# Kernel tuning notes

Measured on AMD Instinct MI355X. Metric: run time of the kernel, lower is better.

Reference implementation:

```python
import jax, jax.numpy as jnp
import numpy as np

N = 50000
E = 800000
IN_DIM = 128
HIDDEN = 32
HEADS = 4
OUT_DIM = 64
NEG_SLOPE = 0.2


def _glorot(key, shape):
    fan_in, fan_out = shape[0], shape[-1]
    lim = jnp.sqrt(6.0 / (fan_in + fan_out))
    return jax.random.uniform(key, shape, jnp.float32, -lim, lim)


def setup_inputs() -> dict:
    key = jax.random.key(0)
    ks = jax.random.split(key, 16)
    x = jax.random.normal(ks[0], (N, IN_DIM), jnp.float32)
    edge_index = jax.random.randint(ks[1], (2, E), 0, N, jnp.int64)
    # layer 0: in_dim -> hidden, heads, concat
    W1 = _glorot(ks[2], (IN_DIM, HEADS * HIDDEN))
    a_src1 = _glorot(ks[3], (HEADS, HIDDEN))
    a_dst1 = _glorot(ks[4], (HEADS, HIDDEN))
    b1 = jnp.zeros((HEADS * HIDDEN,), jnp.float32)
    # layer 1: hidden*heads -> hidden, heads, concat
    W2 = _glorot(ks[5], (HEADS * HIDDEN, HEADS * HIDDEN))
    a_src2 = _glorot(ks[6], (HEADS, HIDDEN))
    a_dst2 = _glorot(ks[7], (HEADS, HIDDEN))
    b2 = jnp.zeros((HEADS * HIDDEN,), jnp.float32)
    # layer 2: hidden*heads -> out_dim, heads, concat=False (mean over heads)
    W3 = _glorot(ks[8], (HEADS * HIDDEN, HEADS * OUT_DIM))
    a_src3 = _glorot(ks[9], (HEADS, OUT_DIM))
    a_dst3 = _glorot(ks[10], (HEADS, OUT_DIM))
    b3 = jnp.zeros((OUT_DIM,), jnp.float32)
    return {"x": x, "edge_index": edge_index,
            "W1": W1, "a_src1": a_src1, "a_dst1": a_dst1, "b1": b1,
            "W2": W2, "a_src2": a_src2, "a_dst2": a_dst2, "b2": b2,
            "W3": W3, "a_src3": a_src3, "a_dst3": a_dst3, "b3": b3}


def gat_conv(x, src, dst, W, a_src, a_dst, bias, out_ch, concat):
    # linear projection, per-head view: [N, H, C]
    h = (x @ W).reshape(N, HEADS, out_ch)
    # per-node attention logits, gathered to edges: [E, H]
    alpha_src = jnp.einsum('nhc,hc->nh', h, a_src)
    alpha_dst = jnp.einsum('nhc,hc->nh', h, a_dst)
    e = jax.nn.leaky_relu(alpha_src[src] + alpha_dst[dst], NEG_SLOPE)
    # segment softmax over incoming edges of each dst node
    m = jax.ops.segment_max(e, dst, num_segments=N)  # [N, H]
    m = jnp.where(jnp.isfinite(m), m, 0.0)
    p = jnp.exp(e - m[dst])  # [E, H]
    denom = jax.ops.segment_sum(p, dst, num_segments=N)  # [N, H]
    alpha = p / (denom[dst] + 1e-16)
    # weighted scatter-add of source features: [N, H, C]
    out = jax.ops.segment_sum(h[src] * alpha[:, :, None], dst, num_segments=N)
    if concat:
        return out.reshape(N, HEADS * out_ch) + bias
    return out.mean(axis=1) + bias


def reference(x, edge_index, W1, a_src1, a_dst1, b1, W2, a_src2, a_dst2, b2,
              W3, a_src3, a_dst3, b3):
    src, dst = edge_index[0], edge_index[1]
    x = gat_conv(x, src, dst, W1, a_src1, a_dst1, b1, HIDDEN, True)
    x = gat_conv(x, src, dst, W2, a_src2, a_dst2, b2, HIDDEN, True)
    x = gat_conv(x, src, dst, W3, a_src3, a_dst3, b3, OUT_DIM, False)
    return x
```

## Files before the change

kernel.cpp:

```cpp
#include <hip/hip_runtime.h>
#include <hip/hip_fp16.h>
#include <math.h>

#define NNODES 50000
#define NEDGES 800000

typedef _Float16 half8 __attribute__((ext_vector_type(8)));
typedef float floatx4 __attribute__((ext_vector_type(4)));


__global__ void zero_i32(int* __restrict__ p, int n) {
    int i = blockIdx.x * 256 + threadIdx.x;
    if (i < n) p[i] = 0;
}

__global__ void hist_kernel(const int* __restrict__ dst, int* __restrict__ counts, int e) {
    int i = blockIdx.x * 256 + threadIdx.x;
    if (i < e) atomicAdd(&counts[dst[i]], 1);
}

__global__ void scan1_kernel(const int* __restrict__ counts, int* __restrict__ row_ptr,
                             int* __restrict__ bsums, int n) {
    __shared__ int s[256];
    int tid = threadIdx.x;
    int i = blockIdx.x * 256 + tid;
    int v = (i < n) ? counts[i] : 0;
    s[tid] = v;
    __syncthreads();
    #pragma unroll
    for (int o = 1; o < 256; o <<= 1) {
        int t = (tid >= o) ? s[tid - o] : 0;
        __syncthreads();
        s[tid] += t;
        __syncthreads();
    }
    if (i < n) row_ptr[i + 1] = s[tid];
    if (tid == 255) bsums[blockIdx.x] = s[255];
}

__global__ void scan2_kernel(int* __restrict__ bsums, int nb) {
    __shared__ int s[256];
    int tid = threadIdx.x;
    int v = (tid < nb) ? bsums[tid] : 0;
    s[tid] = v;
    __syncthreads();
    #pragma unroll
    for (int o = 1; o < 256; o <<= 1) {
        int t = (tid >= o) ? s[tid - o] : 0;
        __syncthreads();
        s[tid] += t;
        __syncthreads();
    }
    if (tid < nb) bsums[tid] = s[tid] - v;
}

__global__ void scan3_kernel(int* __restrict__ row_ptr, const int* __restrict__ bsums,
                             int* __restrict__ cursor, int n) {
    int i = blockIdx.x * 256 + threadIdx.x;
    if (i < n) {
        row_ptr[i + 1] += bsums[blockIdx.x];
        cursor[i] = 0;
    }
    if (i == 0) row_ptr[0] = 0;
}

__global__ void fill_kernel(const int* __restrict__ src, const int* __restrict__ dst,
                            const int* __restrict__ row_ptr, int* __restrict__ cursor,
                            int* __restrict__ csr_src, int e) {
    int i = blockIdx.x * 256 + threadIdx.x;
    if (i < e) {
        int d = dst[i];
        int pos = atomicAdd(&cursor[d], 1);
        csr_src[row_ptr[d] + pos] = src[i];
    }
}


template <int CH, bool AF32, int LAYER>
__global__ __launch_bounds__(256, 3) void gemm_mfma(const void* __restrict__ A_,
                                                    const float* __restrict__ Wf,
                                                    const float* __restrict__ a_src,
                                                    const float* __restrict__ a_dst,
                                                    __half* __restrict__ H,
                                                    float* __restrict__ asrc,
                                                    float* __restrict__ adst, int n, int M) {
    __shared__ __half As[128][136];
    __shared__ __half Ws[64][136];
    float* scrf = (float*)&As[0][0];
    int tid = threadIdx.x;
    int row0 = blockIdx.x * 128;
    int col0 = blockIdx.y * 64;

    if constexpr (AF32) {
        const float* Af = (const float*)A_;
        #pragma unroll
        for (int it = 0; it < 8; ++it) {
            int flat = tid + it * 256;
            int r = flat >> 4;
            int kq = (flat & 15) * 8;
            int gr = row0 + r;
            float4 v0 = {0.f, 0.f, 0.f, 0.f}, v1 = {0.f, 0.f, 0.f, 0.f};
            if (gr < n) {
                v0 = *(const float4*)&Af[(size_t)gr * 128 + kq];
                v1 = *(const float4*)&Af[(size_t)gr * 128 + kq + 4];
            }
            __half2 h0 = __floats2half2_rn(v0.x, v0.y);
            __half2 h1 = __floats2half2_rn(v0.z, v0.w);
            __half2 h2 = __floats2half2_rn(v1.x, v1.y);
            __half2 h3 = __floats2half2_rn(v1.z, v1.w);
            uint4 st = {*(unsigned*)&h0, *(unsigned*)&h1, *(unsigned*)&h2, *(unsigned*)&h3};
            *(uint4*)&As[r][kq] = st;
        }
    } else {
        const __half* Ah = (const __half*)A_;
        #pragma unroll
        for (int it = 0; it < 8; ++it) {
            int flat = tid + it * 256;
            int r = flat >> 4;
            int kq = (flat & 15) * 8;
            int gr = row0 + r;
            float4 v = {0.f, 0.f, 0.f, 0.f};
            if (gr < n) v = *(const float4*)&Ah[(size_t)gr * 128 + kq];
            *(float4*)&As[r][kq] = v;
        }
    }
    #pragma unroll
    for (int it = 0; it < 4; ++it) {
        int flat = tid + it * 256;
        int kp = flat >> 4;
        int c4 = (flat & 15) * 4;
        int k = kp * 2;
        float4 va = *(const float4*)&Wf[(size_t)k * M + col0 + c4];
        float4 vb = *(const float4*)&Wf[(size_t)(k + 1) * M + col0 + c4];
        *(__half2*)&Ws[c4 + 0][k] = __floats2half2_rn(va.x, vb.x);
        *(__half2*)&Ws[c4 + 1][k] = __floats2half2_rn(va.y, vb.y);
        *(__half2*)&Ws[c4 + 2][k] = __floats2half2_rn(va.z, vb.z);
        *(__half2*)&Ws[c4 + 3][k] = __floats2half2_rn(va.w, vb.w);
    }
    __syncthreads();

    int lane = tid & 63;
    int wid = tid >> 6;
    int wm = (wid >> 1) * 64;
    int wn = (wid & 1) * 32;
    int l15 = lane & 15;
    int l4 = lane >> 4;

    floatx4 acc[4][2];
    #pragma unroll
    for (int mf = 0; mf < 4; ++mf)
        #pragma unroll
        for (int nf = 0; nf < 2; ++nf) {
            floatx4 z = {0.f, 0.f, 0.f, 0.f};
            acc[mf][nf] = z;
        }

    #pragma unroll
    for (int ks = 0; ks < 4; ++ks) {
        int kb = ks * 32 + l4 * 8;
        half8 b0 = *(const half8*)&Ws[wn + l15][kb];
        half8 b1 = *(const half8*)&Ws[wn + 16 + l15][kb];
        #pragma unroll
        for (int mf = 0; mf < 4; ++mf) {
            half8 a = *(const half8*)&As[wm + mf * 16 + l15][kb];
            acc[mf][0] = __builtin_amdgcn_mfma_f32_16x16x32_f16(a, b0, acc[mf][0], 0, 0, 0);
            acc[mf][1] = __builtin_amdgcn_mfma_f32_16x16x32_f16(a, b1, acc[mf][1], 0, 0, 0);
        }
    }
    if constexpr (CH == 64) __syncthreads();

    #pragma unroll
    for (int mf = 0; mf < 4; ++mf)
        #pragma unroll
        for (int r = 0; r < 4; ++r) {
            int gr = row0 + wm + mf * 16 + l4 * 4 + r;
            if (gr < n) {
                H[(size_t)gr * M + col0 + wn + l15] = __float2half(acc[mf][0][r]);
                H[(size_t)gr * M + col0 + wn + 16 + l15] = __float2half(acc[mf][1][r]);
            }
        }

    int hw = (col0 + wn) / CH;
    int cb = (col0 + wn) % CH;
    float vs0 = a_src[hw * CH + cb + l15];
    float vs1 = a_src[hw * CH + cb + 16 + l15];
    float vd0 = a_dst[hw * CH + cb + l15];
    float vd1 = a_dst[hw * CH + cb + 16 + l15];

    #pragma unroll
    for (int mf = 0; mf < 4; ++mf)
        #pragma unroll
        for (int r = 0; r < 4; ++r) {
            float ss = acc[mf][0][r] * vs0 + acc[mf][1][r] * vs1;
            float sd = acc[mf][0][r] * vd0 + acc[mf][1][r] * vd1;
            #pragma unroll
            for (int o = 1; o < 16; o <<= 1) {
                ss += __shfl_xor(ss, o);
                sd += __shfl_xor(sd, o);
            }
            if (l15 == 0) {
                int ri = wm + mf * 16 + l4 * 4 + r;
                if constexpr (CH == 32) {
                    int gr = row0 + ri;
                    if (gr < n) {
                        asrc[(size_t)gr * 4 + hw] = ss;
                        adst[(size_t)gr * 4 + hw] = sd;
                    }
                } else {
                    scrf[((wid & 1) * 128 + ri) * 2 + 0] = ss;
                    scrf[((wid & 1) * 128 + ri) * 2 + 1] = sd;
                }
            }
        }
    if constexpr (CH == 64) {
        __syncthreads();
        if (tid < 128) {
            int gr = row0 + tid;
            if (gr < n) {
                int head = col0 / 64;
                asrc[(size_t)gr * 4 + head] = scrf[tid * 2 + 0] + scrf[(128 + tid) * 2 + 0];
                adst[(size_t)gr * 4 + head] = scrf[tid * 2 + 1] + scrf[(128 + tid) * 2 + 1];
            }
        }
    }
}


template <int CPL, bool MEAN, int LAYER>
__global__ __launch_bounds__(256) void aggregate_kernel(
    const __half* __restrict__ h, const float* __restrict__ asrc,
    const float* __restrict__ adst, const int* __restrict__ csr_src,
    const int* __restrict__ row_ptr, const float* __restrict__ bias,
    void* __restrict__ out_, int n) {
    __shared__ float lds[4][332];
    int wid = threadIdx.x >> 6;
    int lane = threadIdx.x & 63;
    int node = blockIdx.x * 4 + wid;
    if (node >= n) return;
    float* Wp = lds[wid];
    int* Ws = (int*)&lds[wid][264];
    int start = row_ptr[node];
    int end = row_ptr[node + 1];
    float4 ad = *(const float4*)&adst[(size_t)node * 4];

    int l32, head, j_off;
    if constexpr (CPL == 2) {
        l32 = lane & 31; head = l32 >> 3; j_off = lane >> 5;
    } else {
        l32 = lane; head = lane >> 4; j_off = 0;
    }
    int hoff = head * 66;

    float acc0 = 0.f, acc1 = 0.f, acc2 = 0.f, acc3 = 0.f, pw = 0.f;

    for (int base = start; base < end; base += 64) {
        int cnt = end - base;
        if (cnt > 64) cnt = 64;
        int s = 0;
        float4 pv = {0.f, 0.f, 0.f, 0.f};
        if (lane < cnt) {
            s = csr_src[base + lane];
            float4 a = *(const float4*)&asrc[(size_t)s * 4];
            float e0 = a.x + ad.x; e0 = (e0 > 0.f) ? e0 : 0.2f * e0;
            float e1 = a.y + ad.y; e1 = (e1 > 0.f) ? e1 : 0.2f * e1;
            float e2 = a.z + ad.z; e2 = (e2 > 0.f) ? e2 : 0.2f * e2;
            float e3 = a.w + ad.w; e3 = (e3 > 0.f) ? e3 : 0.2f * e3;
            pv.x = __expf(e0); pv.y = __expf(e1); pv.z = __expf(e2); pv.w = __expf(e3);
        }
        Wp[0 * 66 + lane] = pv.x;
        Wp[1 * 66 + lane] = pv.y;
        Wp[2 * 66 + lane] = pv.z;
        Wp[3 * 66 + lane] = pv.w;
        Ws[lane] = s;
        __builtin_amdgcn_wave_barrier();
        asm volatile("" ::: "memory");
        if constexpr (CPL == 2) {
            for (int jj = 0; jj < cnt; jj += 16) {
                float w[8]; int sa[8];
                #pragma unroll
                for (int u = 0; u < 8; ++u) {
                    int j = jj + 2 * u + j_off;
                    w[u] = Wp[hoff + j];
                    sa[u] = Ws[j];
                }
                float2 v[8];
                #pragma unroll
                for (int u = 0; u < 8; ++u)
                    v[u] = *(const float2*)(h + (size_t)sa[u] * 128 + l32 * 4);
                #pragma unroll
                for (int u = 0; u < 8; ++u) {
                    float2 f01 = __half22float2(((const __half2*)&v[u])[0]);
                    float2 f23 = __half22float2(((const __half2*)&v[u])[1]);
                    acc0 += w[u] * f01.x;
                    acc1 += w[u] * f01.y;
                    acc2 += w[u] * f23.x;
                    acc3 += w[u] * f23.y;
                    pw += w[u];
                }
            }
        } else {
            for (int jj = 0; jj < cnt; jj += 8) {
                float w[8]; int sa[8];
                #pragma unroll
                for (int u = 0; u < 8; ++u) {
                    int j = jj + u;
                    w[u] = Wp[hoff + j];
                    sa[u] = Ws[j];
                }
                float2 v[8];
                #pragma unroll
                for (int u = 0; u < 8; ++u)
                    v[u] = *(const float2*)(h + (size_t)sa[u] * 256 + lane * 4);
                #pragma unroll
                for (int u = 0; u < 8; ++u) {
                    float2 f01 = __half22float2(((const __half2*)&v[u])[0]);
                    float2 f23 = __half22float2(((const __half2*)&v[u])[1]);
                    acc0 += w[u] * f01.x;
                    acc1 += w[u] * f01.y;
                    acc2 += w[u] * f23.x;
                    acc3 += w[u] * f23.y;
                    pw += w[u];
                }
            }
        }
        __builtin_amdgcn_wave_barrier();
        asm volatile("" ::: "memory");
    }

    if constexpr (!MEAN) {
        acc0 += __shfl_xor(acc0, 32);
        acc1 += __shfl_xor(acc1, 32);
        acc2 += __shfl_xor(acc2, 32);
        acc3 += __shfl_xor(acc3, 32);
        pw += __shfl_xor(pw, 32);
        if (lane < 32) {
            float inv = 1.f / (pw + 1e-16f);
            float4 b = *(const float4*)&bias[l32 * 4];
            __half* out = (__half*)out_;
            __half2 ha = __floats2half2_rn(acc0 * inv + b.x, acc1 * inv + b.y);
            __half2 hb = __floats2half2_rn(acc2 * inv + b.z, acc3 * inv + b.w);
            uint2 st = {*(unsigned int*)&ha, *(unsigned int*)&hb};
            *(uint2*)&out[(size_t)node * 128 + l32 * 4] = st;
        }
    } else {
        float inv = 1.f / (pw + 1e-16f);
        float r0 = acc0 * inv, r1 = acc1 * inv, r2 = acc2 * inv, r3 = acc3 * inv;
        r0 += __shfl_xor(r0, 16); r0 += __shfl_xor(r0, 32);
        r1 += __shfl_xor(r1, 16); r1 += __shfl_xor(r1, 32);
        r2 += __shfl_xor(r2, 16); r2 += __shfl_xor(r2, 32);
        r3 += __shfl_xor(r3, 16); r3 += __shfl_xor(r3, 32);
        if (lane < 16) {
            float* out = (float*)out_;
            float4 b = *(const float4*)&bias[lane * 4];
            float4 o;
            o.x = 0.25f * r0 + b.x;
            o.y = 0.25f * r1 + b.y;
            o.z = 0.25f * r2 + b.z;
            o.w = 0.25f * r3 + b.w;
            *(float4*)&out[(size_t)node * 64 + lane * 4] = o;
        }
    }
}


extern "C" void kernel_launch(void* const* d_in, const int* in_sizes, int n_in,
                              void* d_out, int out_size, void* d_ws, size_t ws_size,
                              hipStream_t stream) {
    const float* x = (const float*)d_in[0];
    const int* ei = (const int*)d_in[1];
    const int* src = ei;
    const int* dst = ei + NEDGES;
    const float* W1 = (const float*)d_in[2];
    const float* as1 = (const float*)d_in[3];
    const float* ad1 = (const float*)d_in[4];
    const float* b1 = (const float*)d_in[5];
    const float* W2 = (const float*)d_in[6];
    const float* as2 = (const float*)d_in[7];
    const float* ad2 = (const float*)d_in[8];
    const float* b2 = (const float*)d_in[9];
    const float* W3 = (const float*)d_in[10];
    const float* as3 = (const float*)d_in[11];
    const float* ad3 = (const float*)d_in[12];
    const float* b3 = (const float*)d_in[13];

    char* ws = (char*)d_ws;
    size_t off = 0;
    auto take = [&](size_t bytes) -> char* {
        char* p = ws + off;
        off = (off + bytes + 255) & ~(size_t)255;
        return p;
    };
    int* csr = (int*)take((size_t)NEDGES * 4);
    int* row_ptr = (int*)take((size_t)(NNODES + 1) * 4);
    int* counts = (int*)take((size_t)NNODES * 4);
    int* cursor = (int*)take((size_t)NNODES * 4);
    int* bsums = (int*)take(1024 * 4);
    float* asrc = (float*)take((size_t)NNODES * 4 * 4);
    float* adst = (float*)take((size_t)NNODES * 4 * 4);
    __half* hbuf = (__half*)take((size_t)NNODES * 256 * 2);
    __half* buf1h = (__half*)take((size_t)NNODES * 128 * 2);
    float* outp = (float*)d_out;

    int nbN = (NNODES + 255) / 256;
    int nbE = (NEDGES + 255) / 256;
    int gnodeAgg = (NNODES + 3) / 4;

    zero_i32<<<nbN, 256, 0, stream>>>(counts, NNODES);
    hist_kernel<<<nbE, 256, 0, stream>>>(dst, counts, NEDGES);
    scan1_kernel<<<nbN, 256, 0, stream>>>(counts, row_ptr, bsums, NNODES);
    scan2_kernel<<<1, 256, 0, stream>>>(bsums, nbN);
    scan3_kernel<<<nbN, 256, 0, stream>>>(row_ptr, bsums, cursor, NNODES);
    fill_kernel<<<nbE, 256, 0, stream>>>(src, dst, row_ptr, cursor, csr, NEDGES);

    dim3 gA((NNODES + 127) / 128, 2);
    dim3 gB((NNODES + 127) / 128, 4);

    gemm_mfma<32, true, 1><<<gA, 256, 0, stream>>>(x, W1, as1, ad1, hbuf, asrc, adst, NNODES, 128);
    aggregate_kernel<2, false, 1><<<gnodeAgg, 256, 0, stream>>>(hbuf, asrc, adst, csr, row_ptr, b1, buf1h, NNODES);

    gemm_mfma<32, false, 2><<<gA, 256, 0, stream>>>(buf1h, W2, as2, ad2, hbuf, asrc, adst, NNODES, 128);
    aggregate_kernel<2, false, 2><<<gnodeAgg, 256, 0, stream>>>(hbuf, asrc, adst, csr, row_ptr, b2, buf1h, NNODES);

    gemm_mfma<64, false, 3><<<gB, 256, 0, stream>>>(buf1h, W3, as3, ad3, hbuf, asrc, adst, NNODES, 256);
    aggregate_kernel<4, true, 3><<<gnodeAgg, 256, 0, stream>>>(hbuf, asrc, adst, csr, row_ptr, b3, outp, NNODES);
}
```

Baseline: 287.2 us.

## Bucket CSR edges by source chunk within each destination row

The CSR build now histograms edges into (destination, source>>12) bins and uses a two-level prefix scan plus a row-pointer extraction kernel. Within each destination row, source indices are therefore grouped by 4096-node chunk. The aim is more local gathers of source features in the aggregation kernels. In exchange, preprocessing now works over about 650k bins and launches several more kernels.

```diff
diff --git a/kernel.cpp b/kernel.cpp
--- a/kernel.cpp
+++ b/kernel.cpp
@@ -4,6 +4,8 @@
 
 #define NNODES 50000
 #define NEDGES 800000
+#define NCHUNK 13
+#define NB2 (NNODES * NCHUNK)
 
 typedef _Float16 half8 __attribute__((ext_vector_type(8)));
 typedef float floatx4 __attribute__((ext_vector_type(4)));
@@ -14,12 +16,13 @@
     if (i < n) p[i] = 0;
 }
 
-__global__ void hist_kernel(const int* __restrict__ dst, int* __restrict__ counts, int e) {
+__global__ void hist2_kernel(const int* __restrict__ src, const int* __restrict__ dst,
+                             int* __restrict__ cnt2, int e) {
     int i = blockIdx.x * 256 + threadIdx.x;
-    if (i < e) atomicAdd(&counts[dst[i]], 1);
-}
-
-__global__ void scan1_kernel(const int* __restrict__ counts, int* __restrict__ row_ptr,
+    if (i < e) atomicAdd(&cnt2[dst[i] * NCHUNK + (src[i] >> 12)], 1);
+}
+
+__global__ void scan1_kernel(const int* __restrict__ counts, int* __restrict__ out,
                              int* __restrict__ bsums, int n) {
     __shared__ int s[256];
     int tid = threadIdx.x;
@@ -34,7 +37,7 @@
         s[tid] += t;
         __syncthreads();
     }
-    if (i < n) row_ptr[i + 1] = s[tid];
+    if (i < n) out[i + 1] = s[tid];
     if (tid == 255) bsums[blockIdx.x] = s[255];
 }
 
@@ -54,24 +57,31 @@
     if (tid < nb) bsums[tid] = s[tid] - v;
 }
 
-__global__ void scan3_kernel(int* __restrict__ row_ptr, const int* __restrict__ bsums,
+__global__ void scan3_kernel(int* __restrict__ out, const int* __restrict__ bsums,
                              int* __restrict__ cursor, int n) {
     int i = blockIdx.x * 256 + threadIdx.x;
     if (i < n) {
-        row_ptr[i + 1] += bsums[blockIdx.x];
+        out[i + 1] += bsums[blockIdx.x];
         cursor[i] = 0;
     }
-    if (i == 0) row_ptr[0] = 0;
-}
-
-__global__ void fill_kernel(const int* __restrict__ src, const int* __restrict__ dst,
-                            const int* __restrict__ row_ptr, int* __restrict__ cursor,
-                            int* __restrict__ csr_src, int e) {
+    if (i == 0) out[0] = 0;
+}
+
+__global__ void rowptr_kernel(const int* __restrict__ cp, int* __restrict__ row_ptr) {
+    int i = blockIdx.x * 256 + threadIdx.x;
+    if (i < NNODES) row_ptr[i] = cp[i * NCHUNK];
+    if (i == NNODES) row_ptr[NNODES] = NEDGES;
+}
+
+__global__ void fill2_kernel(const int* __restrict__ src, const int* __restrict__ dst,
+                             const int* __restrict__ cp, int* __restrict__ cursor,
+                             int* __restrict__ csr_src, int e) {
     int i = blockIdx.x * 256 + threadIdx.x;
     if (i < e) {
-        int d = dst[i];
-        int pos = atomicAdd(&cursor[d], 1);
-        csr_src[row_ptr[d] + pos] = src[i];
+        int s_ = src[i];
+        int b = dst[i] * NCHUNK + (s_ >> 12);
+        int pos = atomicAdd(&cursor[b], 1);
+        csr_src[cp[b] + pos] = s_;
     }
 }
 
@@ -392,25 +402,32 @@
     };
     int* csr = (int*)take((size_t)NEDGES * 4);
     int* row_ptr = (int*)take((size_t)(NNODES + 1) * 4);
-    int* counts = (int*)take((size_t)NNODES * 4);
-    int* cursor = (int*)take((size_t)NNODES * 4);
-    int* bsums = (int*)take(1024 * 4);
+    int* cnt2 = (int*)take((size_t)NB2 * 4);
+    int* cp = (int*)take((size_t)(NB2 + 1) * 4);
+    int* cursor2 = (int*)take((size_t)NB2 * 4);
+    int* bs1 = (int*)take(2608 * 4);
+    int* bs1s = (int*)take(2609 * 4);
+    int* bs2 = (int*)take(64 * 4);
     float* asrc = (float*)take((size_t)NNODES * 4 * 4);
     float* adst = (float*)take((size_t)NNODES * 4 * 4);
     __half* hbuf = (__half*)take((size_t)NNODES * 256 * 2);
     __half* buf1h = (__half*)take((size_t)NNODES * 128 * 2);
     float* outp = (float*)d_out;
 
-    int nbN = (NNODES + 255) / 256;
+    int nbB = (NB2 + 255) / 256;
     int nbE = (NEDGES + 255) / 256;
+    int nb1 = (2540 + 255) / 256;
     int gnodeAgg = (NNODES + 3) / 4;
 
-    zero_i32<<<nbN, 256, 0, stream>>>(counts, NNODES);
-    hist_kernel<<<nbE, 256, 0, stream>>>(dst, counts, NEDGES);
-    scan1_kernel<<<nbN, 256, 0, stream>>>(counts, row_ptr, bsums, NNODES);
-    scan2_kernel<<<1, 256, 0, stream>>>(bsums, nbN);
-    scan3_kernel<<<nbN, 256, 0, stream>>>(row_ptr, bsums, cursor, NNODES);
-    fill_kernel<<<nbE, 256, 0, stream>>>(src, dst, row_ptr, cursor, csr, NEDGES);
+    zero_i32<<<nbB, 256, 0, stream>>>(cnt2, NB2);
+    hist2_kernel<<<nbE, 256, 0, stream>>>(src, dst, cnt2, NEDGES);
+    scan1_kernel<<<nbB, 256, 0, stream>>>(cnt2, cp, bs1, NB2);
+    scan1_kernel<<<nb1, 256, 0, stream>>>(bs1, bs1s, bs2, 2540);
+    scan2_kernel<<<1, 256, 0, stream>>>(bs2, nb1);
+    scan3_kernel<<<nb1, 256, 0, stream>>>(bs1s, bs2, cursor2, 2540);
+    scan3_kernel<<<nbB, 256, 0, stream>>>(cp, bs1s, cursor2, NB2);
+    rowptr_kernel<<<(NNODES + 256) / 256, 256, 0, stream>>>(cp, row_ptr);
+    fill2_kernel<<<nbE, 256, 0, stream>>>(src, dst, cp, cursor2, csr, NEDGES);
 
     dim3 gA((NNODES + 127) / 128, 2);
     dim3 gB((NNODES + 127) / 128, 4);
```

After: 294.4 us. +2.5%, slower.

## Reorder layer-3 GAT as aggregate-then-project using precomputed attention vectors

Applied to the files above, without the earlier changes.

Layer 3 now computes attention logits directly from the 128-dim input with a precombined W3·a vector, skipping the 256-wide projection. It then aggregates the 128-dim input features per head into a 512-wide buffer, and finishes with a single GEMM against a reshaped W3 that also folds in the head mean and bias. The aim is to shrink the per-edge gather width in the last layer (128 fp16 instead of 256 per source) and drop the wide projection. In exchange it writes and reads a 50000x512 fp16 intermediate, adds small weight-prep kernels each call, and changes the fp16 rounding order.

```diff
diff --git a/kernel.cpp b/kernel.cpp
--- a/kernel.cpp
+++ b/kernel.cpp
@@ -75,18 +75,79 @@
     }
 }
 
-
-template <int CH, bool AF32, int LAYER>
+__global__ void prep_v_kernel(const float* __restrict__ W3, const float* __restrict__ as3,
+                              const float* __restrict__ ad3, float* __restrict__ Vs,
+                              float* __restrict__ Vd) {
+    int id = blockIdx.x * 256 + threadIdx.x;
+    if (id >= 1024) return;
+    int which = id >> 9;
+    int rem = id & 511;
+    int k = rem >> 2;
+    int hd = rem & 3;
+    const float* av = which ? ad3 : as3;
+    float s = 0.f;
+    #pragma unroll 8
+    for (int c = 0; c < 64; ++c)
+        s += W3[(size_t)k * 256 + hd * 64 + c] * av[hd * 64 + c];
+    (which ? Vd : Vs)[hd * 128 + k] = s;
+}
+
+__global__ void prep_wr_kernel(const float* __restrict__ W3, __half* __restrict__ Wr) {
+    int id = blockIdx.x * 256 + threadIdx.x;
+    if (id >= 64 * 512) return;
+    int c = id >> 9;
+    int rem = id & 511;
+    int hd = rem >> 7;
+    int k = rem & 127;
+    Wr[(size_t)c * 512 + hd * 128 + k] = __float2half(W3[(size_t)k * 256 + hd * 64 + c]);
+}
+
+__global__ __launch_bounds__(256) void alpha3_kernel(const __half* __restrict__ A,
+                                                     const float* __restrict__ Vs,
+                                                     const float* __restrict__ Vd,
+                                                     float* __restrict__ asrc,
+                                                     float* __restrict__ adst, int n) {
+    int wid = threadIdx.x >> 6;
+    int lane = threadIdx.x & 63;
+    int node = blockIdx.x * 4 + wid;
+    if (node >= n) return;
+    unsigned raw = *(const unsigned*)(A + (size_t)node * 128 + lane * 2);
+    float2 f = __half22float2(*(const __half2*)&raw);
+    float ss[4], sd[4];
+    #pragma unroll
+    for (int hd = 0; hd < 4; ++hd) {
+        ss[hd] = f.x * Vs[hd * 128 + lane * 2] + f.y * Vs[hd * 128 + lane * 2 + 1];
+        sd[hd] = f.x * Vd[hd * 128 + lane * 2] + f.y * Vd[hd * 128 + lane * 2 + 1];
+    }
+    #pragma unroll
+    for (int o = 1; o < 64; o <<= 1) {
+        #pragma unroll
+        for (int hd = 0; hd < 4; ++hd) {
+            ss[hd] += __shfl_xor(ss[hd], o);
+            sd[hd] += __shfl_xor(sd[hd], o);
+        }
+    }
+    if (lane == 0) {
+        #pragma unroll
+        for (int hd = 0; hd < 4; ++hd) {
+            asrc[(size_t)node * 4 + hd] = ss[hd];
+            adst[(size_t)node * 4 + hd] = sd[hd];
+        }
+    }
+}
+
+
+template <bool AF32, int LAYER>
 __global__ __launch_bounds__(256, 3) void gemm_mfma(const void* __restrict__ A_,
                                                     const float* __restrict__ Wf,
                                                     const float* __restrict__ a_src,
                                                     const float* __restrict__ a_dst,
                                                     __half* __restrict__ H,
                                                     float* __restrict__ asrc,
-                                                    float* __restrict__ adst, int n, int M) {
+                                                    float* __restrict__ adst, int n) {
+    const int M = 128, CH = 32;
     __shared__ __half As[128][136];
     __shared__ __half Ws[64][136];
-    float* scrf = (float*)&As[0][0];
     int tid = threadIdx.x;
     int row0 = blockIdx.x * 128;
     int col0 = blockIdx.y * 64;
@@ -167,7 +228,6 @@
             acc[mf][1] = __builtin_amdgcn_mfma_f32_16x16x32_f16(a, b1, acc[mf][1], 0, 0, 0);
         }
     }
-    if constexpr (CH == 64) __syncthreads();
 
     #pragma unroll
     for (int mf = 0; mf < 4; ++mf)
@@ -181,11 +241,10 @@
         }
 
     int hw = (col0 + wn) / CH;
-    int cb = (col0 + wn) % CH;
-    float vs0 = a_src[hw * CH + cb + l15];
-    float vs1 = a_src[hw * CH + cb + 16 + l15];
-    float vd0 = a_dst[hw * CH + cb + l15];
-    float vd1 = a_dst[hw * CH + cb + 16 + l15];
+    float vs0 = a_src[hw * CH + l15];
+    float vs1 = a_src[hw * CH + 16 + l15];
+    float vd0 = a_dst[hw * CH + l15];
+    float vd1 = a_dst[hw * CH + 16 + l15];
 
     #pragma unroll
     for (int mf = 0; mf < 4; ++mf)
@@ -198,40 +257,21 @@
                 ss += __shfl_xor(ss, o);
                 sd += __shfl_xor(sd, o);
             }
-            if (l15 == 0) {
-                int ri = wm + mf * 16 + l4 * 4 + r;
-                if constexpr (CH == 32) {
-                    int gr = row0 + ri;
-                    if (gr < n) {
-                        asrc[(size_t)gr * 4 + hw] = ss;
-                        adst[(size_t)gr * 4 + hw] = sd;
-                    }
-                } else {
-                    scrf[((wid & 1) * 128 + ri) * 2 + 0] = ss;
-                    scrf[((wid & 1) * 128 + ri) * 2 + 1] = sd;
-                }
-            }
-        }
-    if constexpr (CH == 64) {
-        __syncthreads();
-        if (tid < 128) {
-            int gr = row0 + tid;
-            if (gr < n) {
-                int head = col0 / 64;
-                asrc[(size_t)gr * 4 + head] = scrf[tid * 2 + 0] + scrf[(128 + tid) * 2 + 0];
-                adst[(size_t)gr * 4 + head] = scrf[tid * 2 + 1] + scrf[(128 + tid) * 2 + 1];
-            }
-        }
-    }
-}
-
-
-template <int CPL, bool MEAN, int LAYER>
+            int gr = row0 + wm + mf * 16 + l4 * 4 + r;
+            if (l15 == 0 && gr < n) {
+                asrc[(size_t)gr * 4 + hw] = ss;
+                adst[(size_t)gr * 4 + hw] = sd;
+            }
+        }
+}
+
+
+template <int LAYER>
 __global__ __launch_bounds__(256) void aggregate_kernel(
     const __half* __restrict__ h, const float* __restrict__ asrc,
     const float* __restrict__ adst, const int* __restrict__ csr_src,
     const int* __restrict__ row_ptr, const float* __restrict__ bias,
-    void* __restrict__ out_, int n) {
+    __half* __restrict__ out, int n) {
     __shared__ float lds[4][332];
     int wid = threadIdx.x >> 6;
     int lane = threadIdx.x & 63;
@@ -243,12 +283,7 @@
     int end = row_ptr[node + 1];
     float4 ad = *(const float4*)&adst[(size_t)node * 4];
 
-    int l32, head, j_off;
-    if constexpr (CPL == 2) {
-        l32 = lane & 31; head = l32 >> 3; j_off = lane >> 5;
-    } else {
-        l32 = lane; head = lane >> 4; j_off = 0;
-    }
+    int l32 = lane & 31, head = l32 >> 3, j_off = lane >> 5;
     int hoff = head * 66;
 
     float acc0 = 0.f, acc1 = 0.f, acc2 = 0.f, acc3 = 0.f, pw = 0.f;
@@ -274,92 +309,198 @@
         Ws[lane] = s;
         __builtin_amdgcn_wave_barrier();
         asm volatile("" ::: "memory");
-        if constexpr (CPL == 2) {
-            for (int jj = 0; jj < cnt; jj += 16) {
-                float w[8]; int sa[8];
-                #pragma unroll
-                for (int u = 0; u < 8; ++u) {
-                    int j = jj + 2 * u + j_off;
-                    w[u] = Wp[hoff + j];
-                    sa[u] = Ws[j];
-                }
-                float2 v[8];
-                #pragma unroll
-                for (int u = 0; u < 8; ++u)
-                    v[u] = *(const float2*)(h + (size_t)sa[u] * 128 + l32 * 4);
-                #pragma unroll
-                for (int u = 0; u < 8; ++u) {
-                    float2 f01 = __half22float2(((const __half2*)&v[u])[0]);
-                    float2 f23 = __half22float2(((const __half2*)&v[u])[1]);
-                    acc0 += w[u] * f01.x;
-                    acc1 += w[u] * f01.y;
-                    acc2 += w[u] * f23.x;
-                    acc3 += w[u] * f23.y;
-                    pw += w[u];
-                }
-            }
-        } else {
-            for (int jj = 0; jj < cnt; jj += 8) {
-                float w[8]; int sa[8];
-                #pragma unroll
-                for (int u = 0; u < 8; ++u) {
-                    int j = jj + u;
-                    w[u] = Wp[hoff + j];
-                    sa[u] = Ws[j];
-                }
-                float2 v[8];
-                #pragma unroll
-                for (int u = 0; u < 8; ++u)
-                    v[u] = *(const float2*)(h + (size_t)sa[u] * 256 + lane * 4);
-                #pragma unroll
-                for (int u = 0; u < 8; ++u) {
-                    float2 f01 = __half22float2(((const __half2*)&v[u])[0]);
-                    float2 f23 = __half22float2(((const __half2*)&v[u])[1]);
-                    acc0 += w[u] * f01.x;
-                    acc1 += w[u] * f01.y;
-                    acc2 += w[u] * f23.x;
-                    acc3 += w[u] * f23.y;
-                    pw += w[u];
-                }
+        for (int jj = 0; jj < cnt; jj += 16) {
+            float w[8]; int sa[8];
+            #pragma unroll
+            for (int u = 0; u < 8; ++u) {
+                int j = jj + 2 * u + j_off;
+                w[u] = Wp[hoff + j];
+                sa[u] = Ws[j];
+            }
+            float2 v[8];
+            #pragma unroll
+            for (int u = 0; u < 8; ++u)
+                v[u] = *(const float2*)(h + (size_t)sa[u] * 128 + l32 * 4);
+            #pragma unroll
+            for (int u = 0; u < 8; ++u) {
+                float2 f01 = __half22float2(((const __half2*)&v[u])[0]);
+                float2 f23 = __half22float2(((const __half2*)&v[u])[1]);
+                acc0 += w[u] * f01.x;
+                acc1 += w[u] * f01.y;
+                acc2 += w[u] * f23.x;
+                acc3 += w[u] * f23.y;
+                pw += w[u];
             }
         }
         __builtin_amdgcn_wave_barrier();
         asm volatile("" ::: "memory");
     }
 
-    if constexpr (!MEAN) {
-        acc0 += __shfl_xor(acc0, 32);
-        acc1 += __shfl_xor(acc1, 32);
-        acc2 += __shfl_xor(acc2, 32);
-        acc3 += __shfl_xor(acc3, 32);
-        pw += __shfl_xor(pw, 32);
-        if (lane < 32) {
-            float inv = 1.f / (pw + 1e-16f);
-            float4 b = *(const float4*)&bias[l32 * 4];
-            __half* out = (__half*)out_;
-            __half2 ha = __floats2half2_rn(acc0 * inv + b.x, acc1 * inv + b.y);
-            __half2 hb = __floats2half2_rn(acc2 * inv + b.z, acc3 * inv + b.w);
-            uint2 st = {*(unsigned int*)&ha, *(unsigned int*)&hb};
-            *(uint2*)&out[(size_t)node * 128 + l32 * 4] = st;
-        }
-    } else {
+    acc0 += __shfl_xor(acc0, 32);
+    acc1 += __shfl_xor(acc1, 32);
+    acc2 += __shfl_xor(acc2, 32);
+    acc3 += __shfl_xor(acc3, 32);
+    pw += __shfl_xor(pw, 32);
+    if (lane < 32) {
         float inv = 1.f / (pw + 1e-16f);
-        float r0 = acc0 * inv, r1 = acc1 * inv, r2 = acc2 * inv, r3 = acc3 * inv;
-        r0 += __shfl_xor(r0, 16); r0 += __shfl_xor(r0, 32);
-        r1 += __shfl_xor(r1, 16); r1 += __shfl_xor(r1, 32);
-        r2 += __shfl_xor(r2, 16); r2 += __shfl_xor(r2, 32);
-        r3 += __shfl_xor(r3, 16); r3 += __shfl_xor(r3, 32);
-        if (lane < 16) {
-            float* out = (float*)out_;
-            float4 b = *(const float4*)&bias[lane * 4];
-            float4 o;
-            o.x = 0.25f * r0 + b.x;
-            o.y = 0.25f * r1 + b.y;
-            o.z = 0.25f * r2 + b.z;
-            o.w = 0.25f * r3 + b.w;
-            *(float4*)&out[(size_t)node * 64 + lane * 4] = o;
-        }
-    }
+        float4 b = *(const float4*)&bias[l32 * 4];
+        __half2 ha = __floats2half2_rn(acc0 * inv + b.x, acc1 * inv + b.y);
+        __half2 hb = __floats2half2_rn(acc2 * inv + b.z, acc3 * inv + b.w);
+        uint2 st = {*(unsigned int*)&ha, *(unsigned int*)&hb};
+        *(uint2*)&out[(size_t)node * 128 + l32 * 4] = st;
+    }
+}
+
+
+__global__ __launch_bounds__(256) void aggregate_x_kernel(
+    const __half* __restrict__ A, const float* __restrict__ asrc,
+    const float* __restrict__ adst, const int* __restrict__ csr_src,
+    const int* __restrict__ row_ptr, __half* __restrict__ S, int n) {
+    __shared__ float lds[4][320];
+    int wid = threadIdx.x >> 6;
+    int lane = threadIdx.x & 63;
+    int node = blockIdx.x * 4 + wid;
+    if (node >= n) return;
+    float* Wp4 = lds[wid];
+    int* Ws = (int*)&lds[wid][256];
+    int start = row_ptr[node];
+    int end = row_ptr[node + 1];
+    float4 ad = *(const float4*)&adst[(size_t)node * 4];
+
+    float a00 = 0.f, a01 = 0.f, a10 = 0.f, a11 = 0.f;
+    float a20 = 0.f, a21 = 0.f, a30 = 0.f, a31 = 0.f;
+    float4 psum = {0.f, 0.f, 0.f, 0.f};
+
+    for (int base = start; base < end; base += 64) {
+        int cnt = end - base;
+        if (cnt > 64) cnt = 64;
+        int s = 0;
+        float4 pv = {0.f, 0.f, 0.f, 0.f};
+        if (lane < cnt) {
+            s = csr_src[base + lane];
+            float4 a = *(const float4*)&asrc[(size_t)s * 4];
+            float e0 = a.x + ad.x; e0 = (e0 > 0.f) ? e0 : 0.2f * e0;
+            float e1 = a.y + ad.y; e1 = (e1 > 0.f) ? e1 : 0.2f * e1;
+            float e2 = a.z + ad.z; e2 = (e2 > 0.f) ? e2 : 0.2f * e2;
+            float e3 = a.w + ad.w; e3 = (e3 > 0.f) ? e3 : 0.2f * e3;
+            pv.x = __expf(e0); pv.y = __expf(e1); pv.z = __expf(e2); pv.w = __expf(e3);
+            psum.x += pv.x; psum.y += pv.y; psum.z += pv.z; psum.w += pv.w;
+        }
+        *(float4*)&Wp4[lane * 4] = pv;
+        Ws[lane] = s;
+        __builtin_amdgcn_wave_barrier();
+        asm volatile("" ::: "memory");
+        for (int jj = 0; jj < cnt; jj += 8) {
+            int sa[8];
+            #pragma unroll
+            for (int u = 0; u < 8; ++u) sa[u] = Ws[jj + u];
+            unsigned raw[8];
+            #pragma unroll
+            for (int u = 0; u < 8; ++u)
+                raw[u] = *(const unsigned*)(A + (size_t)sa[u] * 128 + lane * 2);
+            #pragma unroll
+            for (int u = 0; u < 8; ++u) {
+                float4 p = *(const float4*)&Wp4[(jj + u) * 4];
+                float2 f = __half22float2(*(const __half2*)&raw[u]);
+                a00 += p.x * f.x; a01 += p.x * f.y;
+                a10 += p.y * f.x; a11 += p.y * f.y;
+                a20 += p.z * f.x; a21 += p.z * f.y;
+                a30 += p.w * f.x; a31 += p.w * f.y;
+            }
+        }
+        __builtin_amdgcn_wave_barrier();
+        asm volatile("" ::: "memory");
+    }
+
+    #pragma unroll
+    for (int o = 1; o < 64; o <<= 1) {
+        psum.x += __shfl_xor(psum.x, o);
+        psum.y += __shfl_xor(psum.y, o);
+        psum.z += __shfl_xor(psum.z, o);
+        psum.w += __shfl_xor(psum.w, o);
+    }
+    float s0 = 0.25f / (psum.x + 1e-16f);
+    float s1 = 0.25f / (psum.y + 1e-16f);
+    float s2 = 0.25f / (psum.z + 1e-16f);
+    float s3 = 0.25f / (psum.w + 1e-16f);
+    size_t sb = (size_t)node * 512 + lane * 2;
+    *(__half2*)&S[sb + 0 * 128] = __floats2half2_rn(a00 * s0, a01 * s0);
+    *(__half2*)&S[sb + 1 * 128] = __floats2half2_rn(a10 * s1, a11 * s1);
+    *(__half2*)&S[sb + 2 * 128] = __floats2half2_rn(a20 * s2, a21 * s2);
+    *(__half2*)&S[sb + 3 * 128] = __floats2half2_rn(a30 * s3, a31 * s3);
+}
+
+
+__global__ __launch_bounds__(256, 3) void post_gemm(const __half* __restrict__ S,
+                                                    const __half* __restrict__ Wr,
+                                                    const float* __restrict__ b3,
+                                                    float* __restrict__ out, int n) {
+    __shared__ __half As[128][136];
+    __shared__ __half Ws[64][136];
+    int tid = threadIdx.x;
+    int row0 = blockIdx.x * 128;
+    int lane = tid & 63;
+    int wid = tid >> 6;
+    int wm = (wid >> 1) * 64;
+    int wn = (wid & 1) * 32;
+    int l15 = lane & 15;
+    int l4 = lane >> 4;
+
+    floatx4 acc[4][2];
+    #pragma unroll
+    for (int mf = 0; mf < 4; ++mf)
+        #pragma unroll
+        for (int nf = 0; nf < 2; ++nf) {
+            floatx4 z = {0.f, 0.f, 0.f, 0.f};
+            acc[mf][nf] = z;
+        }
+
+    for (int kb = 0; kb < 512; kb += 128) {
+        #pragma unroll
+        for (int it = 0; it < 8; ++it) {
+            int flat = tid + it * 256;
+            int r = flat >> 4;
+            int kq = (flat & 15) * 8;
+            int gr = row0 + r;
+            float4 v = {0.f, 0.f, 0.f, 0.f};
+            if (gr < n) v = *(const float4*)&S[(size_t)gr * 512 + kb + kq];
+            *(float4*)&As[r][kq] = v;
+        }
+        #pragma unroll
+        for (int it = 0; it < 4; ++it) {
+            int flat = tid + it * 256;
+            int r = flat >> 4;
+            int kq = (flat & 15) * 8;
+            *(float4*)&Ws[r][kq] = *(const float4*)&Wr[(size_t)r * 512 + kb + kq];
+        }
+        __syncthreads();
+        #pragma unroll
+        for (int ks = 0; ks < 4; ++ks) {
+            int kk = ks * 32 + l4 * 8;
+            half8 b0 = *(const half8*)&Ws[wn + l15][kk];
+            half8 b1 = *(const half8*)&Ws[wn + 16 + l15][kk];
+            #pragma unroll
+            for (int mf = 0; mf < 4; ++mf) {
+                half8 a = *(const half8*)&As[wm + mf * 16 + l15][kk];
+                acc[mf][0] = __builtin_amdgcn_mfma_f32_16x16x32_f16(a, b0, acc[mf][0], 0, 0, 0);
+                acc[mf][1] = __builtin_amdgcn_mfma_f32_16x16x32_f16(a, b1, acc[mf][1], 0, 0, 0);
+            }
+        }
+        __syncthreads();
+    }
+
+    float bl = b3[wn + l15];
+    float bh = b3[wn + 16 + l15];
+    #pragma unroll
+    for (int mf = 0; mf < 4; ++mf)
+        #pragma unroll
+        for (int r = 0; r < 4; ++r) {
+            int gr = row0 + wm + mf * 16 + l4 * 4 + r;
+            if (gr < n) {
+                out[(size_t)gr * 64 + wn + l15] = acc[mf][0][r] + bl;
+                out[(size_t)gr * 64 + wn + 16 + l15] = acc[mf][1][r] + bh;
+            }
+        }
 }
 
 
@@ -397,8 +538,12 @@
     int* bsums = (int*)take(1024 * 4);
     float* asrc = (float*)take((size_t)NNODES * 4 * 4);
     float* adst = (float*)take((size_t)NNODES * 4 * 4);
-    __half* hbuf = (__half*)take((size_t)NNODES * 256 * 2);
+    __half* hbuf = (__half*)take((size_t)NNODES * 128 * 2);
     __half* buf1h = (__half*)take((size_t)NNODES * 128 * 2);
+    __half* Sbuf = (__half*)take((size_t)NNODES * 512 * 2);
+    float* Vs = (float*)take(512 * 4);
+    float* Vd = (float*)take(512 * 4);
+    __half* Wr = (__half*)take((size_t)64 * 512 * 2);
     float* outp = (float*)d_out;
 
     int nbN = (NNODES + 255) / 256;
@@ -411,16 +556,18 @@
     scan2_kernel<<<1, 256, 0, stream>>>(bsums, nbN);
     scan3_kernel<<<nbN, 256, 0, stream>>>(row_ptr, bsums, cursor, NNODES);
     fill_kernel<<<nbE, 256, 0, stream>>>(src, dst, row_ptr, cursor, csr, NEDGES);
+    prep_v_kernel<<<4, 256, 0, stream>>>(W3, as3, ad3, Vs, Vd);
+    prep_wr_kernel<<<128, 256, 0, stream>>>(W3, Wr);
 
     dim3 gA((NNODES + 127) / 128, 2);
-    dim3 gB((NNODES + 127) / 128, 4);
-
-    gemm_mfma<32, true, 1><<<gA, 256, 0, stream>>>(x, W1, as1, ad1, hbuf, asrc, adst, NNODES, 128);
-    aggregate_kernel<2, false, 1><<<gnodeAgg, 256, 0, stream>>>(hbuf, asrc, adst, csr, row_ptr, b1, buf1h, NNODES);
-
-    gemm_mfma<32, false, 2><<<gA, 256, 0, stream>>>(buf1h, W2, as2, ad2, hbuf, asrc, adst, NNODES, 128);
-    aggregate_kernel<2, false, 2><<<gnodeAgg, 256, 0, stream>>>(hbuf, asrc, adst, csr, row_ptr, b2, buf1h, NNODES);
-
-    gemm_mfma<64, false, 3><<<gB, 256, 0, stream>>>(buf1h, W3, as3, ad3, hbuf, asrc, adst, NNODES, 256);
-    aggregate_kernel<4, true, 3><<<gnodeAgg, 256, 0, stream>>>(hbuf, asrc, adst, csr, row_ptr, b3, outp, NNODES);
-}
+
+    gemm_mfma<true, 1><<<gA, 256, 0, stream>>>(x, W1, as1, ad1, hbuf, asrc, adst, NNODES);
+    aggregate_kernel<1><<<gnodeAgg, 256, 0, stream>>>(hbuf, asrc, adst, csr, row_ptr, b1, buf1h, NNODES);
+
+    gemm_mfma<false, 2><<<gA, 256, 0, stream>>>(buf1h, W2, as2, ad2, hbuf, asrc, adst, NNODES);
+    aggregate_kernel<2><<<gnodeAgg, 256, 0, stream>>>(hbuf, asrc, adst, csr, row_ptr, b2, buf1h, NNODES);
+
+    alpha3_kernel<<<gnodeAgg, 256, 0, stream>>>(buf1h, Vs, Vd, asrc, adst, NNODES);
+    aggregate_x_kernel<<<gnodeAgg, 256, 0, stream>>>(buf1h, asrc, adst, csr, row_ptr, Sbuf, NNODES);
+    post_gemm<<<(NNODES + 127) / 128, 256, 0, stream>>>(Sbuf, Wr, b3, outp, NNODES);
+}
```

Result: slower. 297.1 us (+3.4%).
